# Kernel tuning notes

Measured on AMD Instinct MI355X. Metric: run time of the kernel, lower is better.

The kernel has to match this reference:

```python
import jax, jax.numpy as jnp
import numpy as np

B, LQ, LK, E, H, DIM, LAT = 8, 64, 512, 32, 2, 128, 64
DK = E // H


def setup_inputs() -> dict:
    key0 = jax.random.key(0)
    ks = jax.random.split(key0, 10)
    s = 0.05
    return {
        "query": jax.random.normal(ks[0], (B, LQ, E), jnp.float32),
        "key": jax.random.normal(ks[1], (B, LK, E), jnp.float32),
        "value": jax.random.normal(ks[2], (B, LK, DIM), jnp.float32),
        "mask": jax.random.randint(ks[3], (B, LK, DIM), 0, 2, jnp.int32),
        "Wq": jax.random.normal(ks[4], (E, E), jnp.float32) * s,
        "bq": jnp.zeros((E,), jnp.float32),
        "Wk": jax.random.normal(ks[5], (E, E), jnp.float32) * s,
        "bk": jnp.zeros((E,), jnp.float32),
        "Wout": jax.random.normal(ks[6], (DIM * H, LAT), jnp.float32) * s,
        "bout": jnp.zeros((LAT,), jnp.float32),
    }


def reference(query, key, value, mask, Wq, bq, Wk, bk, Wout, bout):
    b, Lk, dim = value.shape
    Lq = query.shape[1]
    # linear query/key maps
    q = query @ Wq + bq              # [b, Lq, E]
    k = key @ Wk + bk                # [b, Lk, E]
    # split heads -> [b, h, L, dk]
    q = q.reshape(b, Lq, H, DK).transpose(0, 2, 1, 3)
    k = k.reshape(b, Lk, H, DK).transpose(0, 2, 1, 3)
    # per-head scores, broadcast over value feature dim (faithful to original)
    scores = jnp.einsum("bhqd,bhkd->bhqk", q, k) / jnp.sqrt(jnp.asarray(DK, q.dtype))
    scores = scores[..., None]                        # [b,h,Lq,Lk,1]
    scores = jnp.where(mask[:, None, None] == 0, -1e9, scores)  # [b,h,Lq,Lk,dim]
    p_attn = jax.nn.softmax(scores, axis=3)           # softmax over Lk per channel
    x = jnp.einsum("bhqkc,bkc->bhqc", p_attn, value)  # [b,h,Lq,dim]
    x = x.transpose(0, 2, 1, 3).reshape(b, Lq, H * dim)
    return x @ Wout + bout            # [b, Lq, LAT]
```

## Files before the change

kernel.cpp:

```cpp
#include <hip/hip_runtime.h>
#include <hip/hip_bf16.h>


#define NBLK 256

__global__ __launch_bounds__(512) void fld_fused(
    const float* __restrict__ query, const float* __restrict__ key,
    const float* __restrict__ value, const int* __restrict__ mask,
    const float* __restrict__ Wq, const float* __restrict__ bq,
    const float* __restrict__ Wk, const float* __restrict__ bk,
    const float* __restrict__ Wout, const float* __restrict__ bout,
    float* __restrict__ out) {
  __shared__ float q_l[2 * 36];
  __shared__ float u_l[4 * 36];
  __shared__ float beta_l[4];
  __shared__ float e_t[2][64 * 4];
  __shared__ float red_n[4 * 8 * 32 * 4];
  __shared__ float red_d[4 * 8 * 32 * 4];
  __shared__ float x_l[2 * 264];
  __shared__ float p4[64 * 64];

  const int tid = threadIdx.x;
  const int blk = blockIdx.x;
  const int b = blk & 7;
  const int q0 = (blk >> 3) * 2;

  if (tid < 64) {
    const int q = tid >> 5, c = tid & 31;
    const float* qrow = query + (size_t)(b * 64 + q0 + q) * 32;
    float acc = bq[c];
#pragma unroll
    for (int t = 0; t < 32; ++t) acc += qrow[t] * Wq[t * 32 + c];
    q_l[q * 36 + c] = acc;
  }
  __syncthreads();
  if (tid < 128) {
    const int row = tid >> 5, t = tid & 31;
    const int h = row >> 1, q = row & 1;
    float acc = 0.f;
#pragma unroll
    for (int c = 0; c < 16; ++c)
      acc += Wk[t * 32 + h * 16 + c] * q_l[q * 36 + h * 16 + c];
    u_l[row * 36 + t] = acc;
  } else if (tid < 132) {
    const int row = tid - 128;
    const int h = row >> 1, q = row & 1;
    float acc = 0.f;
#pragma unroll
    for (int c = 0; c < 16; ++c) acc += bk[h * 16 + c] * q_l[q * 36 + h * 16 + c];
    beta_l[row] = acc;
  }
  __syncthreads();

  float u_reg[32];
  float beta_reg = 0.f;
  if (tid < 256) {
    const int row = tid >> 6;
#pragma unroll
    for (int i = 0; i < 8; ++i) {
      float4 v = *(const float4*)&u_l[row * 36 + i * 4];
      u_reg[i * 4 + 0] = v.x; u_reg[i * 4 + 1] = v.y;
      u_reg[i * 4 + 2] = v.z; u_reg[i * 4 + 3] = v.w;
    }
    beta_reg = beta_l[tid >> 6];
  }

  auto do_scores = [&](int kc, int buf) {
    if (tid < 256) {
      const int row = tid >> 6, k = tid & 63;
      const float* krow = key + (size_t)(b * 512 + kc * 64 + k) * 32;
      float acc = beta_reg;
#pragma unroll
      for (int i = 0; i < 8; ++i) {
        float4 v = *(const float4*)&krow[i * 4];
        acc += u_reg[i * 4 + 0] * v.x + u_reg[i * 4 + 1] * v.y +
               u_reg[i * 4 + 2] * v.z + u_reg[i * 4 + 3] * v.w;
      }
      e_t[buf][k * 4 + row] = __expf(acc * 0.25f);
    }
  };

  float n_acc[4][4] = {}, d_acc[4][4] = {};
  const int w = tid >> 6, kkl = (tid >> 5) & 1, cq = tid & 31;
  const int kb = w * 2 + kkl;
  const float4* value4 = (const float4*)value;
  const int4* mask4 = (const int4*)mask;

  do_scores(0, 0);
  for (int kc = 0; kc < 8; ++kc) {
    __syncthreads();
    if (kc + 1 < 8) do_scores(kc + 1, (kc + 1) & 1);
#pragma unroll
    for (int j = 0; j < 4; ++j) {
      const int kk = kb + j * 16;
      const size_t g = (size_t)(b * 512 + kc * 64 + kk) * 32 + cq;
      float4 v = value4[g];
      int4 mm = mask4[g];
      float4 e4 = *(const float4*)&e_t[kc & 1][kk * 4];
      float ev[4] = {e4.x, e4.y, e4.z, e4.w};
      float mv[4], mk[4];
      mv[0] = mm.x ? v.x : 0.f; mk[0] = mm.x ? 1.f : 0.f;
      mv[1] = mm.y ? v.y : 0.f; mk[1] = mm.y ? 1.f : 0.f;
      mv[2] = mm.z ? v.z : 0.f; mk[2] = mm.z ? 1.f : 0.f;
      mv[3] = mm.w ? v.w : 0.f; mk[3] = mm.w ? 1.f : 0.f;
#pragma unroll
      for (int r = 0; r < 4; ++r) {
#pragma unroll
        for (int i = 0; i < 4; ++i) {
          n_acc[r][i] += ev[r] * mv[i];
          d_acc[r][i] += ev[r] * mk[i];
        }
      }
    }
  }

#pragma unroll
  for (int r = 0; r < 4; ++r)
#pragma unroll
    for (int i = 0; i < 4; ++i) {
      n_acc[r][i] += __shfl_xor(n_acc[r][i], 32);
      d_acc[r][i] += __shfl_xor(d_acc[r][i], 32);
    }
  if ((tid & 32) == 0) {
#pragma unroll
    for (int r = 0; r < 4; ++r) {
      float4 nn, dd;
      nn.x = n_acc[r][0]; nn.y = n_acc[r][1]; nn.z = n_acc[r][2]; nn.w = n_acc[r][3];
      dd.x = d_acc[r][0]; dd.y = d_acc[r][1]; dd.z = d_acc[r][2]; dd.w = d_acc[r][3];
      *(float4*)&red_n[((r * 8 + w) * 32 + cq) * 4] = nn;
      *(float4*)&red_d[((r * 8 + w) * 32 + cq) * 4] = dd;
    }
  }
  __syncthreads();
  if (tid < 128) {
    const int r = tid >> 5, c = tid & 31;
    float4 ns = {0.f, 0.f, 0.f, 0.f}, ds = {0.f, 0.f, 0.f, 0.f};
#pragma unroll
    for (int g = 0; g < 8; ++g) {
      float4 nn = *(const float4*)&red_n[((r * 8 + g) * 32 + c) * 4];
      float4 dd = *(const float4*)&red_d[((r * 8 + g) * 32 + c) * 4];
      ns.x += nn.x; ns.y += nn.y; ns.z += nn.z; ns.w += nn.w;
      ds.x += dd.x; ds.y += dd.y; ds.z += dd.z; ds.w += dd.w;
    }
    const int h = r >> 1, q = r & 1;
    float4 x;
    x.x = ns.x / ds.x; x.y = ns.y / ds.y; x.z = ns.z / ds.z; x.w = ns.w / ds.w;
    *(float4*)&x_l[q * 264 + h * 128 + c * 4] = x;
  }
  __syncthreads();

  {
    const int g = tid >> 4, oc4 = tid & 15;
    float4 a0 = {0.f, 0.f, 0.f, 0.f}, a1 = {0.f, 0.f, 0.f, 0.f};
#pragma unroll
    for (int j = 0; j < 8; ++j) {
      const int k = g * 8 + j;
      float4 w4 = *(const float4*)&Wout[k * 64 + oc4 * 4];
      const float xv0 = x_l[k];
      const float xv1 = x_l[264 + k];
      a0.x += xv0 * w4.x; a0.y += xv0 * w4.y; a0.z += xv0 * w4.z; a0.w += xv0 * w4.w;
      a1.x += xv1 * w4.x; a1.y += xv1 * w4.y; a1.z += xv1 * w4.z; a1.w += xv1 * w4.w;
    }
    *(float4*)&p4[(g * 2 + 0) * 64 + oc4 * 4] = a0;
    *(float4*)&p4[(g * 2 + 1) * 64 + oc4 * 4] = a1;
  }
  __syncthreads();
  if (tid < 128) {
    const int q = tid >> 6, oc = tid & 63;
    float acc = bout[oc];
#pragma unroll
    for (int g = 0; g < 32; ++g) acc += p4[(g * 2 + q) * 64 + oc];
    out[(size_t)(b * 64 + q0 + q) * 64 + oc] = acc;
  }
}

extern "C" void kernel_launch(void* const* d_in, const int* in_sizes, int n_in,
                              void* d_out, int out_size, void* d_ws, size_t ws_size,
                              hipStream_t stream) {
  const float* query = (const float*)d_in[0];
  const float* key   = (const float*)d_in[1];
  const float* value = (const float*)d_in[2];
  const int*   mask  = (const int*)d_in[3];
  const float* Wq    = (const float*)d_in[4];
  const float* bq    = (const float*)d_in[5];
  const float* Wk    = (const float*)d_in[6];
  const float* bk    = (const float*)d_in[7];
  const float* Wout  = (const float*)d_in[8];
  const float* bout  = (const float*)d_in[9];
  float* out = (float*)d_out;

  fld_fused<<<NBLK, 512, 0, stream>>>(query, key, value, mask, Wq, bq, Wk, bk,
                                      Wout, bout, out);
}
```

Measured before the change: 93.66 us.

## Prefetch value/mask tiles into registers and alternate score work across half-blocks

Value and mask loads for the next key chunk are now issued into a register double buffer before the barrier, and the first chunk's loads start before the projection prologue. Global load latency can then overlap with the score computation and the accumulation of the current chunk. Score computation alternates between the lower and upper 256 threads by chunk parity, which spreads that work across more waves. The cost is much higher register pressure from two sets of float4/int4 buffers plus a fully unrolled loop, which could reduce occupancy.

Measured after the change: 136.3 us. 45.5% more time.

```diff
diff --git a/kernel.cpp b/kernel.cpp
--- a/kernel.cpp
+++ b/kernel.cpp
@@ -25,6 +25,26 @@
   const int b = blk & 7;
   const int q0 = (blk >> 3) * 2;
 
+  const int w = tid >> 6, kkl = (tid >> 5) & 1, cq = tid & 31;
+  const int kb = w * 2 + kkl;
+  const int row4 = (tid >> 6) & 3;
+  const float4* value4 = (const float4*)value;
+  const int4* mask4 = (const int4*)mask;
+
+  auto issue = [&](int kc, float4 (&pv)[4], int4 (&pm)[4]) {
+#pragma unroll
+    for (int j = 0; j < 4; ++j) {
+      const int kk = kb + j * 16;
+      const size_t g = (size_t)(b * 512 + kc * 64 + kk) * 32 + cq;
+      pv[j] = value4[g];
+      pm[j] = mask4[g];
+    }
+  };
+
+  float4 pv0[4], pv1[4];
+  int4 pm0[4], pm1[4];
+  issue(0, pv0, pm0);
+
   if (tid < 64) {
     const int q = tid >> 5, c = tid & 31;
     const float* qrow = query + (size_t)(b * 64 + q0 + q) * 32;
@@ -53,21 +73,17 @@
   __syncthreads();
 
   float u_reg[32];
-  float beta_reg = 0.f;
-  if (tid < 256) {
-    const int row = tid >> 6;
-#pragma unroll
-    for (int i = 0; i < 8; ++i) {
-      float4 v = *(const float4*)&u_l[row * 36 + i * 4];
-      u_reg[i * 4 + 0] = v.x; u_reg[i * 4 + 1] = v.y;
-      u_reg[i * 4 + 2] = v.z; u_reg[i * 4 + 3] = v.w;
-    }
-    beta_reg = beta_l[tid >> 6];
-  }
-
-  auto do_scores = [&](int kc, int buf) {
-    if (tid < 256) {
-      const int row = tid >> 6, k = tid & 63;
+#pragma unroll
+  for (int i = 0; i < 8; ++i) {
+    float4 v = *(const float4*)&u_l[row4 * 36 + i * 4];
+    u_reg[i * 4 + 0] = v.x; u_reg[i * 4 + 1] = v.y;
+    u_reg[i * 4 + 2] = v.z; u_reg[i * 4 + 3] = v.w;
+  }
+  const float beta_reg = beta_l[row4];
+
+  auto do_scores = [&](int kc) {
+    if ((tid >> 8) == (kc & 1)) {
+      const int k = tid & 63;
       const float* krow = key + (size_t)(b * 512 + kc * 64 + k) * 32;
       float acc = beta_reg;
 #pragma unroll
@@ -76,41 +92,48 @@
         acc += u_reg[i * 4 + 0] * v.x + u_reg[i * 4 + 1] * v.y +
                u_reg[i * 4 + 2] * v.z + u_reg[i * 4 + 3] * v.w;
       }
-      e_t[buf][k * 4 + row] = __expf(acc * 0.25f);
+      e_t[kc & 1][k * 4 + row4] = __expf(acc * 0.25f);
     }
   };
 
   float n_acc[4][4] = {}, d_acc[4][4] = {};
-  const int w = tid >> 6, kkl = (tid >> 5) & 1, cq = tid & 31;
-  const int kb = w * 2 + kkl;
-  const float4* value4 = (const float4*)value;
-  const int4* mask4 = (const int4*)mask;
-
-  do_scores(0, 0);
-  for (int kc = 0; kc < 8; ++kc) {
-    __syncthreads();
-    if (kc + 1 < 8) do_scores(kc + 1, (kc + 1) & 1);
+  auto accum = [&](const float4 (&pv)[4], const int4 (&pm)[4], int buf) {
 #pragma unroll
     for (int j = 0; j < 4; ++j) {
       const int kk = kb + j * 16;
-      const size_t g = (size_t)(b * 512 + kc * 64 + kk) * 32 + cq;
-      float4 v = value4[g];
-      int4 mm = mask4[g];
-      float4 e4 = *(const float4*)&e_t[kc & 1][kk * 4];
+      float4 e4 = *(const float4*)&e_t[buf][kk * 4];
       float ev[4] = {e4.x, e4.y, e4.z, e4.w};
+      const float4 v = pv[j];
+      const int4 mm = pm[j];
       float mv[4], mk[4];
       mv[0] = mm.x ? v.x : 0.f; mk[0] = mm.x ? 1.f : 0.f;
       mv[1] = mm.y ? v.y : 0.f; mk[1] = mm.y ? 1.f : 0.f;
       mv[2] = mm.z ? v.z : 0.f; mk[2] = mm.z ? 1.f : 0.f;
       mv[3] = mm.w ? v.w : 0.f; mk[3] = mm.w ? 1.f : 0.f;
 #pragma unroll
-      for (int r = 0; r < 4; ++r) {
+      for (int r = 0; r < 4; ++r)
 #pragma unroll
         for (int i = 0; i < 4; ++i) {
           n_acc[r][i] += ev[r] * mv[i];
           d_acc[r][i] += ev[r] * mk[i];
         }
-      }
+    }
+  };
+
+  do_scores(0);
+
+#pragma unroll
+  for (int kc = 0; kc < 8; ++kc) {
+    if ((kc & 1) == 0) {
+      if (kc + 1 < 8) issue(kc + 1, pv1, pm1);
+      __syncthreads();
+      if (kc + 1 < 8) do_scores(kc + 1);
+      accum(pv0, pm0, 0);
+    } else {
+      if (kc + 1 < 8) issue(kc + 1, pv0, pm0);
+      __syncthreads();
+      if (kc + 1 < 8) do_scores(kc + 1);
+      accum(pv1, pm1, 1);
     }
   }
 
```

## Software-pipeline value/mask loads with register double buffering and split score work

Applied to the files above, without the earlier changes.

Fully unrolls the key-chunk loop and prefetches the next chunk's value and mask vectors into a second register set before the barrier, so global loads overlap with accumulation. The first chunk's loads are issued at kernel start, ahead of the query projection. Score computation now alternates between the two halves of the block by chunk parity instead of always using the first 256 threads. Launch bounds now request two blocks per SM, which may limit registers while the live register count grows.

New measurement: 135.7 us. +44.9%, slower.

```diff
diff --git a/kernel.cpp b/kernel.cpp
--- a/kernel.cpp
+++ b/kernel.cpp
@@ -4,7 +4,7 @@
 
 #define NBLK 256
 
-__global__ __launch_bounds__(512) void fld_fused(
+__global__ __launch_bounds__(512, 2) void fld_fused(
     const float* __restrict__ query, const float* __restrict__ key,
     const float* __restrict__ value, const int* __restrict__ mask,
     const float* __restrict__ Wq, const float* __restrict__ bq,
@@ -25,6 +25,68 @@
   const int b = blk & 7;
   const int q0 = (blk >> 3) * 2;
 
+  const int w = tid >> 6, kkl = (tid >> 5) & 1, cq = tid & 31;
+  const int kb = w * 2 + kkl;
+  const int row4 = (tid >> 6) & 3;
+  const float4* vb = (const float4*)value + (size_t)b * 512 * 32;
+  const int4* mb = (const int4*)mask + (size_t)b * 512 * 32;
+
+  float4 vA0, vA1, vA2, vA3, vB0, vB1, vB2, vB3;
+  int4 mA0, mA1, mA2, mA3, mB0, mB1, mB2, mB3;
+
+#define ISSUE(V0, V1, V2, V3, M0, M1, M2, M3, kc)      \
+  do {                                                 \
+    V0 = vb[((kc) * 64 + kb + 0) * 32 + cq];           \
+    M0 = mb[((kc) * 64 + kb + 0) * 32 + cq];           \
+    V1 = vb[((kc) * 64 + kb + 16) * 32 + cq];          \
+    M1 = mb[((kc) * 64 + kb + 16) * 32 + cq];          \
+    V2 = vb[((kc) * 64 + kb + 32) * 32 + cq];          \
+    M2 = mb[((kc) * 64 + kb + 32) * 32 + cq];          \
+    V3 = vb[((kc) * 64 + kb + 48) * 32 + cq];          \
+    M3 = mb[((kc) * 64 + kb + 48) * 32 + cq];          \
+  } while (0)
+
+#define DO_SCORES(kc)                                                   \
+  do {                                                                  \
+    if ((tid >> 8) == ((kc) & 1)) {                                     \
+      const int k_ = tid & 63;                                          \
+      const float* krow_ = key + (size_t)(b * 512 + (kc) * 64 + k_) * 32; \
+      float acc_ = beta_reg;                                            \
+      _Pragma("unroll") for (int i_ = 0; i_ < 8; ++i_) {                \
+        float4 v_ = *(const float4*)&krow_[i_ * 4];                     \
+        acc_ += u_reg[i_ * 4 + 0] * v_.x + u_reg[i_ * 4 + 1] * v_.y +   \
+                u_reg[i_ * 4 + 2] * v_.z + u_reg[i_ * 4 + 3] * v_.w;    \
+      }                                                                 \
+      e_t[(kc) & 1][k_ * 4 + row4] = __expf(acc_ * 0.25f);              \
+    }                                                                   \
+  } while (0)
+
+#define ACC1(V, M, jj, ebuf)                                            \
+  do {                                                                  \
+    float4 e4_ = *(const float4*)&e_t[ebuf][(kb + (jj) * 16) * 4];      \
+    float ev_[4] = {e4_.x, e4_.y, e4_.z, e4_.w};                        \
+    float mv_[4], mk_[4];                                               \
+    mv_[0] = M.x ? V.x : 0.f; mk_[0] = M.x ? 1.f : 0.f;                 \
+    mv_[1] = M.y ? V.y : 0.f; mk_[1] = M.y ? 1.f : 0.f;                 \
+    mv_[2] = M.z ? V.z : 0.f; mk_[2] = M.z ? 1.f : 0.f;                 \
+    mv_[3] = M.w ? V.w : 0.f; mk_[3] = M.w ? 1.f : 0.f;                 \
+    _Pragma("unroll") for (int r_ = 0; r_ < 4; ++r_)                    \
+      _Pragma("unroll") for (int i_ = 0; i_ < 4; ++i_) {                \
+        n_acc[r_][i_] += ev_[r_] * mv_[i_];                             \
+        d_acc[r_][i_] += ev_[r_] * mk_[i_];                             \
+      }                                                                 \
+  } while (0)
+
+#define ACCUM(V0, V1, V2, V3, M0, M1, M2, M3, ebuf) \
+  do {                                              \
+    ACC1(V0, M0, 0, ebuf);                          \
+    ACC1(V1, M1, 1, ebuf);                          \
+    ACC1(V2, M2, 2, ebuf);                          \
+    ACC1(V3, M3, 3, ebuf);                          \
+  } while (0)
+
+  ISSUE(vA0, vA1, vA2, vA3, mA0, mA1, mA2, mA3, 0);
+
   if (tid < 64) {
     const int q = tid >> 5, c = tid & 31;
     const float* qrow = query + (size_t)(b * 64 + q0 + q) * 32;
@@ -53,66 +115,55 @@
   __syncthreads();
 
   float u_reg[32];
-  float beta_reg = 0.f;
-  if (tid < 256) {
-    const int row = tid >> 6;
-#pragma unroll
-    for (int i = 0; i < 8; ++i) {
-      float4 v = *(const float4*)&u_l[row * 36 + i * 4];
-      u_reg[i * 4 + 0] = v.x; u_reg[i * 4 + 1] = v.y;
-      u_reg[i * 4 + 2] = v.z; u_reg[i * 4 + 3] = v.w;
-    }
-    beta_reg = beta_l[tid >> 6];
-  }
-
-  auto do_scores = [&](int kc, int buf) {
-    if (tid < 256) {
-      const int row = tid >> 6, k = tid & 63;
-      const float* krow = key + (size_t)(b * 512 + kc * 64 + k) * 32;
-      float acc = beta_reg;
-#pragma unroll
-      for (int i = 0; i < 8; ++i) {
-        float4 v = *(const float4*)&krow[i * 4];
-        acc += u_reg[i * 4 + 0] * v.x + u_reg[i * 4 + 1] * v.y +
-               u_reg[i * 4 + 2] * v.z + u_reg[i * 4 + 3] * v.w;
-      }
-      e_t[buf][k * 4 + row] = __expf(acc * 0.25f);
-    }
-  };
+#pragma unroll
+  for (int i = 0; i < 8; ++i) {
+    float4 v = *(const float4*)&u_l[row4 * 36 + i * 4];
+    u_reg[i * 4 + 0] = v.x; u_reg[i * 4 + 1] = v.y;
+    u_reg[i * 4 + 2] = v.z; u_reg[i * 4 + 3] = v.w;
+  }
+  const float beta_reg = beta_l[row4];
 
   float n_acc[4][4] = {}, d_acc[4][4] = {};
-  const int w = tid >> 6, kkl = (tid >> 5) & 1, cq = tid & 31;
-  const int kb = w * 2 + kkl;
-  const float4* value4 = (const float4*)value;
-  const int4* mask4 = (const int4*)mask;
-
-  do_scores(0, 0);
-  for (int kc = 0; kc < 8; ++kc) {
-    __syncthreads();
-    if (kc + 1 < 8) do_scores(kc + 1, (kc + 1) & 1);
-#pragma unroll
-    for (int j = 0; j < 4; ++j) {
-      const int kk = kb + j * 16;
-      const size_t g = (size_t)(b * 512 + kc * 64 + kk) * 32 + cq;
-      float4 v = value4[g];
-      int4 mm = mask4[g];
-      float4 e4 = *(const float4*)&e_t[kc & 1][kk * 4];
-      float ev[4] = {e4.x, e4.y, e4.z, e4.w};
-      float mv[4], mk[4];
-      mv[0] = mm.x ? v.x : 0.f; mk[0] = mm.x ? 1.f : 0.f;
-      mv[1] = mm.y ? v.y : 0.f; mk[1] = mm.y ? 1.f : 0.f;
-      mv[2] = mm.z ? v.z : 0.f; mk[2] = mm.z ? 1.f : 0.f;
-      mv[3] = mm.w ? v.w : 0.f; mk[3] = mm.w ? 1.f : 0.f;
-#pragma unroll
-      for (int r = 0; r < 4; ++r) {
-#pragma unroll
-        for (int i = 0; i < 4; ++i) {
-          n_acc[r][i] += ev[r] * mv[i];
-          d_acc[r][i] += ev[r] * mk[i];
-        }
-      }
-    }
-  }
+
+  DO_SCORES(0);
+
+  ISSUE(vB0, vB1, vB2, vB3, mB0, mB1, mB2, mB3, 1);
+  __syncthreads();
+  DO_SCORES(1);
+  ACCUM(vA0, vA1, vA2, vA3, mA0, mA1, mA2, mA3, 0);
+
+  ISSUE(vA0, vA1, vA2, vA3, mA0, mA1, mA2, mA3, 2);
+  __syncthreads();
+  DO_SCORES(2);
+  ACCUM(vB0, vB1, vB2, vB3, mB0, mB1, mB2, mB3, 1);
+
+  ISSUE(vB0, vB1, vB2, vB3, mB0, mB1, mB2, mB3, 3);
+  __syncthreads();
+  DO_SCORES(3);
+  ACCUM(vA0, vA1, vA2, vA3, mA0, mA1, mA2, mA3, 0);
+
+  ISSUE(vA0, vA1, vA2, vA3, mA0, mA1, mA2, mA3, 4);
+  __syncthreads();
+  DO_SCORES(4);
+  ACCUM(vB0, vB1, vB2, vB3, mB0, mB1, mB2, mB3, 1);
+
+  ISSUE(vB0, vB1, vB2, vB3, mB0, mB1, mB2, mB3, 5);
+  __syncthreads();
+  DO_SCORES(5);
+  ACCUM(vA0, vA1, vA2, vA3, mA0, mA1, mA2, mA3, 0);
+
+  ISSUE(vA0, vA1, vA2, vA3, mA0, mA1, mA2, mA3, 6);
+  __syncthreads();
+  DO_SCORES(6);
+  ACCUM(vB0, vB1, vB2, vB3, mB0, mB1, mB2, mB3, 1);
+
+  ISSUE(vB0, vB1, vB2, vB3, mB0, mB1, mB2, mB3, 7);
+  __syncthreads();
+  DO_SCORES(7);
+  ACCUM(vA0, vA1, vA2, vA3, mA0, mA1, mA2, mA3, 0);
+
+  __syncthreads();
+  ACCUM(vB0, vB1, vB2, vB3, mB0, mB1, mB2, mB3, 1);
 
 #pragma unroll
   for (int r = 0; r < 4; ++r)
```

## Compute all 512 key scores up front, then run a single sync-free accumulation loop

Applied to the files above, without the earlier changes.

All 512 threads now compute the exp-scores for every key of the batch in one pass, each thread handling one key row, and store them in a full shared buffer. This replaces the chunked double-buffered scheme, in which only half the threads did score work and a barrier ran per 64-key chunk. The value/mask accumulation then runs as one 32-iteration loop with partial unrolling and no barriers, which removes 8 block syncs. In exchange, the key loads no longer overlap with value streaming, and shared memory for the score buffer grows to 8 KB.

Result: faster. 83.89 us (-10.4%).

```diff
diff --git a/kernel.cpp b/kernel.cpp
--- a/kernel.cpp
+++ b/kernel.cpp
@@ -14,7 +14,7 @@
   __shared__ float q_l[2 * 36];
   __shared__ float u_l[4 * 36];
   __shared__ float beta_l[4];
-  __shared__ float e_t[2][64 * 4];
+  __shared__ float e_t[512 * 4];
   __shared__ float red_n[4 * 8 * 32 * 4];
   __shared__ float red_d[4 * 8 * 32 * 4];
   __shared__ float x_l[2 * 264];
@@ -52,66 +52,75 @@
   }
   __syncthreads();
 
-  float u_reg[32];
-  float beta_reg = 0.f;
-  if (tid < 256) {
-    const int row = tid >> 6;
-#pragma unroll
-    for (int i = 0; i < 8; ++i) {
-      float4 v = *(const float4*)&u_l[row * 36 + i * 4];
-      u_reg[i * 4 + 0] = v.x; u_reg[i * 4 + 1] = v.y;
-      u_reg[i * 4 + 2] = v.z; u_reg[i * 4 + 3] = v.w;
-    }
-    beta_reg = beta_l[tid >> 6];
-  }
-
-  auto do_scores = [&](int kc, int buf) {
-    if (tid < 256) {
-      const int row = tid >> 6, k = tid & 63;
-      const float* krow = key + (size_t)(b * 512 + kc * 64 + k) * 32;
-      float acc = beta_reg;
-#pragma unroll
-      for (int i = 0; i < 8; ++i) {
-        float4 v = *(const float4*)&krow[i * 4];
-        acc += u_reg[i * 4 + 0] * v.x + u_reg[i * 4 + 1] * v.y +
-               u_reg[i * 4 + 2] * v.z + u_reg[i * 4 + 3] * v.w;
-      }
-      e_t[buf][k * 4 + row] = __expf(acc * 0.25f);
-    }
-  };
-
-  float n_acc[4][4] = {}, d_acc[4][4] = {};
+  {
+    const int k = tid;
+    const float* krow = key + (size_t)(b * 512 + k) * 32;
+    const float4 k0 = *(const float4*)&krow[0];
+    const float4 k1 = *(const float4*)&krow[4];
+    const float4 k2 = *(const float4*)&krow[8];
+    const float4 k3 = *(const float4*)&krow[12];
+    const float4 k4 = *(const float4*)&krow[16];
+    const float4 k5 = *(const float4*)&krow[20];
+    const float4 k6 = *(const float4*)&krow[24];
+    const float4 k7 = *(const float4*)&krow[28];
+    float s[4];
+#pragma unroll
+    for (int r = 0; r < 4; ++r) {
+      float acc = beta_l[r];
+      const float* ur = &u_l[r * 36];
+      float4 u4;
+      u4 = *(const float4*)&ur[0];
+      acc += u4.x * k0.x + u4.y * k0.y + u4.z * k0.z + u4.w * k0.w;
+      u4 = *(const float4*)&ur[4];
+      acc += u4.x * k1.x + u4.y * k1.y + u4.z * k1.z + u4.w * k1.w;
+      u4 = *(const float4*)&ur[8];
+      acc += u4.x * k2.x + u4.y * k2.y + u4.z * k2.z + u4.w * k2.w;
+      u4 = *(const float4*)&ur[12];
+      acc += u4.x * k3.x + u4.y * k3.y + u4.z * k3.z + u4.w * k3.w;
+      u4 = *(const float4*)&ur[16];
+      acc += u4.x * k4.x + u4.y * k4.y + u4.z * k4.z + u4.w * k4.w;
+      u4 = *(const float4*)&ur[20];
+      acc += u4.x * k5.x + u4.y * k5.y + u4.z * k5.z + u4.w * k5.w;
+      u4 = *(const float4*)&ur[24];
+      acc += u4.x * k6.x + u4.y * k6.y + u4.z * k6.z + u4.w * k6.w;
+      u4 = *(const float4*)&ur[28];
+      acc += u4.x * k7.x + u4.y * k7.y + u4.z * k7.z + u4.w * k7.w;
+      s[r] = acc;
+    }
+    float4 er;
+    er.x = __expf(s[0] * 0.25f);
+    er.y = __expf(s[1] * 0.25f);
+    er.z = __expf(s[2] * 0.25f);
+    er.w = __expf(s[3] * 0.25f);
+    *(float4*)&e_t[k * 4] = er;
+  }
+  __syncthreads();
+
   const int w = tid >> 6, kkl = (tid >> 5) & 1, cq = tid & 31;
   const int kb = w * 2 + kkl;
-  const float4* value4 = (const float4*)value;
-  const int4* mask4 = (const int4*)mask;
-
-  do_scores(0, 0);
-  for (int kc = 0; kc < 8; ++kc) {
-    __syncthreads();
-    if (kc + 1 < 8) do_scores(kc + 1, (kc + 1) & 1);
-#pragma unroll
-    for (int j = 0; j < 4; ++j) {
-      const int kk = kb + j * 16;
-      const size_t g = (size_t)(b * 512 + kc * 64 + kk) * 32 + cq;
-      float4 v = value4[g];
-      int4 mm = mask4[g];
-      float4 e4 = *(const float4*)&e_t[kc & 1][kk * 4];
-      float ev[4] = {e4.x, e4.y, e4.z, e4.w};
-      float mv[4], mk[4];
-      mv[0] = mm.x ? v.x : 0.f; mk[0] = mm.x ? 1.f : 0.f;
-      mv[1] = mm.y ? v.y : 0.f; mk[1] = mm.y ? 1.f : 0.f;
-      mv[2] = mm.z ? v.z : 0.f; mk[2] = mm.z ? 1.f : 0.f;
-      mv[3] = mm.w ? v.w : 0.f; mk[3] = mm.w ? 1.f : 0.f;
-#pragma unroll
-      for (int r = 0; r < 4; ++r) {
-#pragma unroll
-        for (int i = 0; i < 4; ++i) {
-          n_acc[r][i] += ev[r] * mv[i];
-          d_acc[r][i] += ev[r] * mk[i];
-        }
+  float n_acc[4][4] = {}, d_acc[4][4] = {};
+  const float4* vb = (const float4*)value + (size_t)b * 512 * 32;
+  const int4* mb = (const int4*)mask + (size_t)b * 512 * 32;
+
+#pragma unroll 4
+  for (int j = 0; j < 32; ++j) {
+    const int kk = kb + j * 16;
+    const float4 v = vb[kk * 32 + cq];
+    const int4 mm = mb[kk * 32 + cq];
+    const float4 e4 = *(const float4*)&e_t[kk * 4];
+    float ev[4] = {e4.x, e4.y, e4.z, e4.w};
+    float mv[4], mk[4];
+    mv[0] = mm.x ? v.x : 0.f; mk[0] = mm.x ? 1.f : 0.f;
+    mv[1] = mm.y ? v.y : 0.f; mk[1] = mm.y ? 1.f : 0.f;
+    mv[2] = mm.z ? v.z : 0.f; mk[2] = mm.z ? 1.f : 0.f;
+    mv[3] = mm.w ? v.w : 0.f; mk[3] = mm.w ? 1.f : 0.f;
+#pragma unroll
+    for (int r = 0; r < 4; ++r)
+#pragma unroll
+      for (int i = 0; i < 4; ++i) {
+        n_acc[r][i] += ev[r] * mv[i];
+        d_acc[r][i] += ev[r] * mk[i];
       }
-    }
   }
 
 #pragma unroll
```
